# Optimization experiments

Measured on AMD Instinct MI355X. Metric: run time of the kernel, lower is better.

## Reference

```python
import jax, jax.numpy as jnp
import numpy as np

N, C, H, W, SF = 4, 3, 1024, 1024, 4


def setup_inputs() -> dict:
    key = jax.random.key(0)
    ks = jax.random.split(key, 6)
    z = jax.random.normal(ks[0], (N, C, H, W), dtype=jnp.float32)
    Fk = jax.random.normal(ks[1], (N, C, H, W, 2), dtype=jnp.float32)
    FkC = jax.random.normal(ks[2], (N, C, H, W, 2), dtype=jnp.float32)
    F2k = jax.random.normal(ks[3], (N, C, H, W, 2), dtype=jnp.float32)
    FkCFy = jax.random.normal(ks[4], (N, C, H, W, 2), dtype=jnp.float32)
    # alpha is a positive penalty weight; keep it away from 0 (it divides FX)
    alpha = jax.random.uniform(ks[5], (N, 1, 1, 1), dtype=jnp.float32,
                               minval=0.1, maxval=1.0)
    return {"z": z, "Fk": Fk, "FkC": FkC, "F2k": F2k,
            "FkCFy": FkCFy, "alpha": alpha, "sf": SF}


def _toc(t):
    # [..., 2] real/imag pair (old torch.rfft onesided=False layout) -> complex
    return jax.lax.complex(t[..., 0], t[..., 1])


def _block_mean(a, sf):
    # torch splits() + mean over the sf*sf blocks == mean over an sf-strided
    # block decomposition of the H and W axes (order of blocks is irrelevant
    # under the mean). a: (N, C, H, W) complex -> (N, C, H//sf, W//sf)
    n, c, h, w = a.shape
    return a.reshape(n, c, sf, h // sf, sf, w // sf).mean(axis=(2, 4))


def reference(z, Fk, FkC, F2k, FkCFy, alpha, sf):
    # torch.rfft(x, 2, onesided=False) == full 2-D FFT over last two dims
    FR = _toc(FkCFy) + jnp.fft.fft2(alpha * z)                  # (N,C,H,W) complex
    FBR = _block_mean(_toc(Fk) * FR, sf)                        # (N,C,H/sf,W/sf)
    invW = _block_mean(_toc(F2k), sf)                           # (N,C,H/sf,W/sf)
    invWBR = FBR / (invW + alpha)                               # csum adds alpha to real part
    FCBinvWBR = _toc(FkC) * jnp.tile(invWBR, (1, 1, sf, sf))    # torch .repeat == tile
    FX = (FR - FCBinvWBR) / alpha
    # torch.irfft(FX, 2, onesided=False) == real part of inverse 2-D FFT
    return jnp.real(jnp.fft.ifft2(FX))
```

## Files before the change

### kernel.cpp

```cpp
#include <hip/hip_runtime.h>
#include <cmath>

#define HN 1024
#define NCH 12
#define PI2 6.28318530717958647692f

__device__ __forceinline__ float2 cmul(float2 a, float2 b) {
  return make_float2(a.x * b.x - a.y * b.y, a.x * b.y + a.y * b.x);
}

__device__ __forceinline__ int drev(int k) {
  int r = 0;
#pragma unroll
  for (int i = 0; i < 5; ++i) { r = (r << 2) | (k & 3); k >>= 2; }
  return r;
}

__device__ __forceinline__ int aswz(int h, int w) { return w ^ ((h & 63) << 4); }

#define RIDX(h) ((h) + ((h) >> 4))
#define TIDX(i) ((i) + ((i) >> 4))
#define EIDX(h, c) ((h) * 17 + (c))

template <bool INV>
__device__ __forceinline__ void bf4(float2& a0, float2& a1, float2& a2, float2& a3,
                                    const float2* tw, int e) {
  float2 t0 = make_float2(a0.x + a2.x, a0.y + a2.y);
  float2 t1 = make_float2(a0.x - a2.x, a0.y - a2.y);
  float2 t2 = make_float2(a1.x + a3.x, a1.y + a3.y);
  float2 t3 = make_float2(a1.x - a3.x, a1.y - a3.y);
  float2 b0 = make_float2(t0.x + t2.x, t0.y + t2.y);
  float2 b2 = make_float2(t0.x - t2.x, t0.y - t2.y);
  float2 b1, b3;
  if (!INV) {
    b1 = make_float2(t1.x + t3.y, t1.y - t3.x);
    b3 = make_float2(t1.x - t3.y, t1.y + t3.x);
  } else {
    b1 = make_float2(t1.x - t3.y, t1.y + t3.x);
    b3 = make_float2(t1.x + t3.y, t1.y - t3.x);
  }
  float2 w1 = tw[e], w2 = tw[2 * e], w3 = tw[3 * e];
  if (INV) { w1.y = -w1.y; w2.y = -w2.y; w3.y = -w3.y; }
  a0 = b0;
  a1 = cmul(b1, w1);
  a2 = cmul(b2, w2);
  a3 = cmul(b3, w3);
}

template <bool INV>
__device__ __forceinline__ void bf4t(float2& a0, float2& a1, float2& a2, float2& a3,
                                     const float2* tw, int e) {
  float2 t0 = make_float2(a0.x + a2.x, a0.y + a2.y);
  float2 t1 = make_float2(a0.x - a2.x, a0.y - a2.y);
  float2 t2 = make_float2(a1.x + a3.x, a1.y + a3.y);
  float2 t3 = make_float2(a1.x - a3.x, a1.y - a3.y);
  float2 b0 = make_float2(t0.x + t2.x, t0.y + t2.y);
  float2 b2 = make_float2(t0.x - t2.x, t0.y - t2.y);
  float2 b1, b3;
  if (!INV) {
    b1 = make_float2(t1.x + t3.y, t1.y - t3.x);
    b3 = make_float2(t1.x - t3.y, t1.y + t3.x);
  } else {
    b1 = make_float2(t1.x - t3.y, t1.y + t3.x);
    b3 = make_float2(t1.x + t3.y, t1.y - t3.x);
  }
  float2 w1 = tw[TIDX(e)], w2 = tw[TIDX(2 * e)], w3 = tw[TIDX(3 * e)];
  if (INV) { w1.y = -w1.y; w2.y = -w2.y; w3.y = -w3.y; }
  a0 = b0;
  a1 = cmul(b1, w1);
  a2 = cmul(b2, w2);
  a3 = cmul(b3, w3);
}

__device__ __forceinline__ void tw_init(float2* tw, int t, int nthr) {
  for (int i = t; i < 768; i += nthr) {
    float s, c;
    sincosf((float)i * (PI2 / 1024.f), &s, &c);
    tw[i] = make_float2(c, -s);
  }
}

__device__ __forceinline__ void tw_init_p(float2* tw, int t, int nthr) {
  for (int i = t; i < 768; i += nthr) {
    float s, c;
    sincosf((float)i * (PI2 / 1024.f), &s, &c);
    tw[TIDX(i)] = make_float2(c, -s);
  }
}

template <bool INV>
__device__ __forceinline__ void fft_row(float2* x, const float2* tw, int t) {
#pragma unroll
  for (int ld = 8; ld >= 0; ld -= 2) {
    __syncthreads();
    const int d = 1 << ld;
    int j = t & (d - 1);
    int p0 = ((t >> ld) << (ld + 2)) | j;
    float2 a0 = x[RIDX(p0)];
    float2 a1 = x[RIDX(p0 + d)];
    float2 a2 = x[RIDX(p0 + 2 * d)];
    float2 a3 = x[RIDX(p0 + 3 * d)];
    bf4<INV>(a0, a1, a2, a3, tw, j << (8 - ld));
    x[RIDX(p0)] = a0;
    x[RIDX(p0 + d)] = a1;
    x[RIDX(p0 + 2 * d)] = a2;
    x[RIDX(p0 + 3 * d)] = a3;
  }
  __syncthreads();
}

template <bool INV>
__device__ __forceinline__ void colfft16(float2 (&r)[16], float2 (&q)[16],
                                         float2* ex, const float2* tw,
                                         int u, int c) {
  const int j2 = u & 3, B = u >> 2;
#pragma unroll
  for (int s = 0; s < 4; ++s)
    bf4t<INV>(r[s], r[s + 4], r[s + 8], r[s + 12], tw, u + (s << 6));
#pragma unroll
  for (int g = 0; g < 4; ++g)
    bf4t<INV>(r[4 * g], r[4 * g + 1], r[4 * g + 2], r[4 * g + 3], tw, u << 2);
#pragma unroll
  for (int it = 0; it < 8; ++it)
    ex[EIDX(u + (it << 6), c)] = r[it];
  __syncthreads();
  if (u < 32) {
#pragma unroll
    for (int m = 0; m < 16; ++m) {
      int hl = (B << 6) + j2 + ((m & 3) << 2) + ((m >> 2) << 4);
      q[m] = ex[EIDX(hl, c)];
    }
  }
  __syncthreads();
#pragma unroll
  for (int it = 8; it < 16; ++it)
    ex[EIDX(u + (it << 6) - 512, c)] = r[it];
  __syncthreads();
  if (u >= 32) {
#pragma unroll
    for (int m = 0; m < 16; ++m) {
      int hl = ((B - 8) << 6) + j2 + ((m & 3) << 2) + ((m >> 2) << 4);
      q[m] = ex[EIDX(hl, c)];
    }
  }
#pragma unroll
  for (int a = 0; a < 4; ++a)
    bf4t<INV>(q[a], q[4 + a], q[8 + a], q[12 + a], tw, (j2 + 4 * a) << 4);
#pragma unroll
  for (int b_ = 0; b_ < 4; ++b_)
    bf4t<INV>(q[4 * b_], q[4 * b_ + 1], q[4 * b_ + 2], q[4 * b_ + 3], tw, j2 << 6);
#pragma unroll
  for (int m = 0; m < 16; ++m) {
    float2 v = q[m];
    float2 p;
    p.x = __shfl_xor(v.x, 32);
    p.y = __shfl_xor(v.y, 32);
    float2 w;
    if (j2 & 2) { w.x = p.x - v.x; w.y = p.y - v.y; }
    else        { w.x = v.x + p.x; w.y = v.y + p.y; }
    float2 p2;
    p2.x = __shfl_xor(w.x, 16);
    p2.y = __shfl_xor(w.y, 16);
    float2 o;
    if (j2 == 0)      { o = make_float2(w.x + p2.x, w.y + p2.y); }
    else if (j2 == 1) { o = make_float2(p2.x - w.x, p2.y - w.y); }
    else if (j2 == 2) { o = INV ? make_float2(w.x - p2.y, w.y + p2.x)
                                : make_float2(w.x + p2.y, w.y - p2.x); }
    else              { o = INV ? make_float2(p2.x + w.y, p2.y - w.x)
                                : make_float2(p2.x - w.y, p2.y + w.x); }
    q[m] = o;
  }
}

__global__ __launch_bounds__(256) void k1_rowfft(const float* __restrict__ z,
                                                 const float* __restrict__ alpha,
                                                 float2* __restrict__ A) {
  __shared__ float2 x[1088];
  __shared__ float2 tw[768];
  const int t = threadIdx.x;
  const int row = blockIdx.x, nc = blockIdx.y;
  tw_init(tw, t, 256);
  const float al = alpha[nc / 3];
  const float* zr = z + ((size_t)nc * HN + row) * HN;
#pragma unroll
  for (int it = 0; it < 4; ++it) {
    int h = t + (it << 8);
    x[RIDX(h)] = make_float2(zr[h] * al, 0.f);
  }
  fft_row<false>(x, tw, t);
  float2* Ar = A + (size_t)nc * HN * HN + (size_t)row * HN;
  const int X = (row & 63) << 4;
#pragma unroll
  for (int it = 0; it < 4; ++it) {
    int k = t + (it << 8);
    Ar[k ^ X] = x[RIDX(drev(k))];
  }
}

__global__ __launch_bounds__(1024, 4) void k2_colfft(float2* __restrict__ A,
                                                     const float2* __restrict__ FkCFy) {
  __shared__ float2 ex[8704];
  __shared__ float2 tw[816];
  const int t = threadIdx.x;
  const int c = t & 15, u = t >> 4;
  const int w0 = blockIdx.x << 4;
  const int nc = blockIdx.y;
  const size_t base = (size_t)nc * HN * HN;
  float2 r[16], q[16];
#pragma unroll
  for (int it = 0; it < 16; ++it) {
    int h = u + (it << 6);
    r[it] = A[base + (size_t)h * HN + (aswz(h, w0) + c)];
  }
  tw_init_p(tw, t, 1024);
  __syncthreads();
  colfft16<false>(r, q, ex, tw, u, c);
  const int j2 = u & 3, B = u >> 2;
  const int f = ((j2 & 1) << 1) | (j2 >> 1);
#pragma unroll
  for (int m = 0; m < 16; ++m) {
    int k = (f << 8) | ((m & 3) << 6) | ((m >> 2) << 4) | ((B & 3) << 2) | (B >> 2);
    float2 fy = FkCFy[base + (size_t)k * HN + w0 + c];
    A[base + (size_t)k * HN + (aswz(k, w0) + c)] =
        make_float2(q[m].x + fy.x, q[m].y + fy.y);
  }
}

__global__ __launch_bounds__(256) void k3_reduce(const float2* __restrict__ A,
                                                 const float2* __restrict__ Fk,
                                                 const float2* __restrict__ F2k,
                                                 const float* __restrict__ alpha,
                                                 float2* __restrict__ iw) {
  int idx = blockIdx.x * 256 + threadIdx.x;
  int j = idx & 255, i = (idx >> 8) & 255, nc = idx >> 16;
  size_t base = (size_t)nc * HN * HN;
  float sx = 0.f, sy = 0.f, wx = 0.f, wy = 0.f;
#pragma unroll
  for (int s1 = 0; s1 < 4; ++s1) {
#pragma unroll
    for (int s2 = 0; s2 < 4; ++s2) {
      int h = (s1 << 8) + i, w = (s2 << 8) + j;
      size_t gl = base + (size_t)h * HN + w;
      float2 fr = A[base + (size_t)h * HN + aswz(h, w)];
      float2 fk = Fk[gl];
      float2 f2 = F2k[gl];
      sx += fk.x * fr.x - fk.y * fr.y;
      sy += fk.x * fr.y + fk.y * fr.x;
      wx += f2.x;
      wy += f2.y;
    }
  }
  const float al = alpha[nc / 3];
  float dx = wx * 0.0625f + al, dy = wy * 0.0625f;
  float nx = sx * 0.0625f, ny = sy * 0.0625f;
  float inv = 1.0f / (dx * dx + dy * dy);
  iw[idx] = make_float2((nx * dx + ny * dy) * inv, (ny * dx - nx * dy) * inv);
}

__global__ __launch_bounds__(1024, 4) void k4_colifft(float2* __restrict__ A,
                                                      const float2* __restrict__ FkC,
                                                      const float2* __restrict__ iw,
                                                      const float* __restrict__ alpha) {
  __shared__ float2 ex[8704];
  __shared__ float2 tw[816];
  const int t = threadIdx.x;
  const int c = t & 15, u = t >> 4;
  const int w0 = blockIdx.x << 4;
  const int nc = blockIdx.y;
  const float al = alpha[nc / 3];
  const float ra = 1.0f / al;
  const size_t base = (size_t)nc * HN * HN;
  const int jcol = (w0 + c) & 255;
  const float2* iwp = iw + ((size_t)nc << 16);
  float2 r[16], q[16];
#pragma unroll
  for (int it = 0; it < 16; ++it) {
    int h = u + (it << 6);
    float2 fr = A[base + (size_t)h * HN + (aswz(h, w0) + c)];
    float2 fc = FkC[base + (size_t)h * HN + w0 + c];
    float2 w = iwp[((h & 255) << 8) | jcol];
    float2 p = cmul(fc, w);
    r[it] = make_float2((fr.x - p.x) * ra, (fr.y - p.y) * ra);
  }
  tw_init_p(tw, t, 1024);
  __syncthreads();
  colfft16<true>(r, q, ex, tw, u, c);
  const int j2 = u & 3, B = u >> 2;
  const int f = ((j2 & 1) << 1) | (j2 >> 1);
#pragma unroll
  for (int m = 0; m < 16; ++m) {
    int k = (f << 8) | ((m & 3) << 6) | ((m >> 2) << 4) | ((B & 3) << 2) | (B >> 2);
    A[base + (size_t)k * HN + (aswz(k, w0) + c)] = q[m];
  }
}

__global__ __launch_bounds__(256) void k5_rowifft(const float2* __restrict__ A,
                                                  float* __restrict__ out) {
  __shared__ float2 x[1088];
  __shared__ float2 tw[768];
  const int t = threadIdx.x;
  const int row = blockIdx.x, nc = blockIdx.y;
  tw_init(tw, t, 256);
  const float2* Ar = A + (size_t)nc * HN * HN + (size_t)row * HN;
  const int X = (row & 63) << 4;
#pragma unroll
  for (int it = 0; it < 4; ++it) {
    int h = t + (it << 8);
    x[RIDX(h)] = Ar[h ^ X];
  }
  fft_row<true>(x, tw, t);
  float* outr = out + ((size_t)nc * HN + row) * HN;
  const float sc = 1.0f / (1024.0f * 1024.0f);
#pragma unroll
  for (int it = 0; it < 4; ++it) {
    int k = t + (it << 8);
    outr[k] = x[RIDX(drev(k))].x * sc;
  }
}

extern "C" void kernel_launch(void* const* d_in, const int* in_sizes, int n_in,
                              void* d_out, int out_size, void* d_ws, size_t ws_size,
                              hipStream_t stream) {
  const float*  z      = (const float*)d_in[0];
  const float2* Fk     = (const float2*)d_in[1];
  const float2* FkC    = (const float2*)d_in[2];
  const float2* F2k    = (const float2*)d_in[3];
  const float2* FkCFy  = (const float2*)d_in[4];
  const float*  alpha  = (const float*)d_in[5];
  (void)in_sizes; (void)n_in; (void)out_size; (void)ws_size;

  float2* A  = (float2*)d_ws;
  float2* iw = A + (size_t)NCH * HN * HN;
  float*  out = (float*)d_out;

  k1_rowfft<<<dim3(HN, NCH), dim3(256), 0, stream>>>(z, alpha, A);
  k2_colfft<<<dim3(HN / 16, NCH), dim3(1024), 0, stream>>>(A, FkCFy);
  k3_reduce<<<dim3(NCH * 256), dim3(256), 0, stream>>>(A, Fk, F2k, alpha, iw);
  k4_colifft<<<dim3(HN / 16, NCH), dim3(1024), 0, stream>>>(A, FkC, iw, alpha);
  k5_rowifft<<<dim3(HN, NCH), dim3(256), 0, stream>>>(A, out);
}
```

Baseline: 278.1 us.

## Fuse Fk*FR partial block reduction into column FFT and vectorize row I/O

The column FFT kernel now multiplies each FR value by Fk and partially reduces it across the four sf-strided row blocks with wave shuffles. It writes the partial sums to a small workspace buffer P, so the reduce kernel no longer re-reads the full FR and Fk arrays. The row FFT kernels also switch their global loads and stores to float4 accesses. This trades extra shuffles and Fk reads inside the column kernel for much less traffic in the reduce kernel. It also relies on extra workspace being available past iw.

```diff
diff --git a/kernel.cpp b/kernel.cpp
--- a/kernel.cpp
+++ b/kernel.cpp
@@ -181,24 +181,31 @@
   const int row = blockIdx.x, nc = blockIdx.y;
   tw_init(tw, t, 256);
   const float al = alpha[nc / 3];
-  const float* zr = z + ((size_t)nc * HN + row) * HN;
-#pragma unroll
-  for (int it = 0; it < 4; ++it) {
-    int h = t + (it << 8);
-    x[RIDX(h)] = make_float2(zr[h] * al, 0.f);
+  const float4* zr4 = (const float4*)(z + ((size_t)nc * HN + row) * HN);
+  {
+    float4 v = zr4[t];
+    int h = t << 2;
+    x[RIDX(h + 0)] = make_float2(v.x * al, 0.f);
+    x[RIDX(h + 1)] = make_float2(v.y * al, 0.f);
+    x[RIDX(h + 2)] = make_float2(v.z * al, 0.f);
+    x[RIDX(h + 3)] = make_float2(v.w * al, 0.f);
   }
   fft_row<false>(x, tw, t);
-  float2* Ar = A + (size_t)nc * HN * HN + (size_t)row * HN;
+  float4* Ar4 = (float4*)(A + (size_t)nc * HN * HN + (size_t)row * HN);
   const int X = (row & 63) << 4;
 #pragma unroll
-  for (int it = 0; it < 4; ++it) {
-    int k = t + (it << 8);
-    Ar[k ^ X] = x[RIDX(drev(k))];
+  for (int half = 0; half < 2; ++half) {
+    int k0 = (half << 9) | (t << 1);
+    float2 a = x[RIDX(drev(k0))];
+    float2 b = x[RIDX(drev(k0 | 1))];
+    Ar4[(k0 ^ X) >> 1] = make_float4(a.x, a.y, b.x, b.y);
   }
 }
 
 __global__ __launch_bounds__(1024, 4) void k2_colfft(float2* __restrict__ A,
-                                                     const float2* __restrict__ FkCFy) {
+                                                     const float2* __restrict__ FkCFy,
+                                                     const float2* __restrict__ Fk,
+                                                     float2* __restrict__ P) {
   __shared__ float2 ex[8704];
   __shared__ float2 tw[816];
   const int t = threadIdx.x;
@@ -217,38 +224,48 @@
   colfft16<false>(r, q, ex, tw, u, c);
   const int j2 = u & 3, B = u >> 2;
   const int f = ((j2 & 1) << 1) | (j2 >> 1);
+  float2* Pp = P + (((size_t)nc) << 18) + w0 + c;
 #pragma unroll
   for (int m = 0; m < 16; ++m) {
-    int k = (f << 8) | ((m & 3) << 6) | ((m >> 2) << 4) | ((B & 3) << 2) | (B >> 2);
+    int klo = ((m & 3) << 6) | ((m >> 2) << 4) | ((B & 3) << 2) | (B >> 2);
+    int k = (f << 8) | klo;
     float2 fy = FkCFy[base + (size_t)k * HN + w0 + c];
-    A[base + (size_t)k * HN + (aswz(k, w0) + c)] =
-        make_float2(q[m].x + fy.x, q[m].y + fy.y);
-  }
-}
-
-__global__ __launch_bounds__(256) void k3_reduce(const float2* __restrict__ A,
-                                                 const float2* __restrict__ Fk,
+    float2 fr = make_float2(q[m].x + fy.x, q[m].y + fy.y);
+    A[base + (size_t)k * HN + (aswz(k, w0) + c)] = fr;
+    float2 fk = Fk[base + (size_t)k * HN + w0 + c];
+    float2 pr = cmul(fk, fr);
+    pr.x += __shfl_xor(pr.x, 16);
+    pr.y += __shfl_xor(pr.y, 16);
+    pr.x += __shfl_xor(pr.x, 32);
+    pr.y += __shfl_xor(pr.y, 32);
+    if (j2 == 0) Pp[(size_t)klo << 10] = pr;
+  }
+}
+
+__global__ __launch_bounds__(256) void k3_reduce(const float2* __restrict__ P,
                                                  const float2* __restrict__ F2k,
                                                  const float* __restrict__ alpha,
                                                  float2* __restrict__ iw) {
   int idx = blockIdx.x * 256 + threadIdx.x;
   int j = idx & 255, i = (idx >> 8) & 255, nc = idx >> 16;
   size_t base = (size_t)nc * HN * HN;
-  float sx = 0.f, sy = 0.f, wx = 0.f, wy = 0.f;
+  float wx = 0.f, wy = 0.f;
 #pragma unroll
   for (int s1 = 0; s1 < 4; ++s1) {
 #pragma unroll
     for (int s2 = 0; s2 < 4; ++s2) {
-      int h = (s1 << 8) + i, w = (s2 << 8) + j;
-      size_t gl = base + (size_t)h * HN + w;
-      float2 fr = A[base + (size_t)h * HN + aswz(h, w)];
-      float2 fk = Fk[gl];
-      float2 f2 = F2k[gl];
-      sx += fk.x * fr.x - fk.y * fr.y;
-      sy += fk.x * fr.y + fk.y * fr.x;
+      float2 f2 = F2k[base + (size_t)((s1 << 8) + i) * HN + ((s2 << 8) + j)];
       wx += f2.x;
       wy += f2.y;
     }
+  }
+  const float2* Pp = P + (((size_t)nc) << 18) + ((size_t)i << 10);
+  float sx = 0.f, sy = 0.f;
+#pragma unroll
+  for (int s2 = 0; s2 < 4; ++s2) {
+    float2 p = Pp[(s2 << 8) + j];
+    sx += p.x;
+    sy += p.y;
   }
   const float al = alpha[nc / 3];
   float dx = wx * 0.0625f + al, dy = wy * 0.0625f;
@@ -301,20 +318,26 @@
   const int t = threadIdx.x;
   const int row = blockIdx.x, nc = blockIdx.y;
   tw_init(tw, t, 256);
-  const float2* Ar = A + (size_t)nc * HN * HN + (size_t)row * HN;
+  const float4* Ar4 = (const float4*)(A + (size_t)nc * HN * HN + (size_t)row * HN);
   const int X = (row & 63) << 4;
 #pragma unroll
-  for (int it = 0; it < 4; ++it) {
-    int h = t + (it << 8);
-    x[RIDX(h)] = Ar[h ^ X];
+  for (int half = 0; half < 2; ++half) {
+    int h0 = (half << 9) | (t << 1);
+    float4 v = Ar4[(h0 ^ X) >> 1];
+    x[RIDX(h0)] = make_float2(v.x, v.y);
+    x[RIDX(h0 | 1)] = make_float2(v.z, v.w);
   }
   fft_row<true>(x, tw, t);
-  float* outr = out + ((size_t)nc * HN + row) * HN;
+  float4* outr4 = (float4*)(out + ((size_t)nc * HN + row) * HN);
   const float sc = 1.0f / (1024.0f * 1024.0f);
-#pragma unroll
-  for (int it = 0; it < 4; ++it) {
-    int k = t + (it << 8);
-    outr[k] = x[RIDX(drev(k))].x * sc;
+  {
+    int k = t << 2;
+    float4 o;
+    o.x = x[RIDX(drev(k + 0))].x * sc;
+    o.y = x[RIDX(drev(k + 1))].x * sc;
+    o.z = x[RIDX(drev(k + 2))].x * sc;
+    o.w = x[RIDX(drev(k + 3))].x * sc;
+    outr4[t] = o;
   }
 }
 
@@ -331,11 +354,12 @@
 
   float2* A  = (float2*)d_ws;
   float2* iw = A + (size_t)NCH * HN * HN;
+  float2* P  = iw + (size_t)NCH * 256 * 256;
   float*  out = (float*)d_out;
 
   k1_rowfft<<<dim3(HN, NCH), dim3(256), 0, stream>>>(z, alpha, A);
-  k2_colfft<<<dim3(HN / 16, NCH), dim3(1024), 0, stream>>>(A, FkCFy);
-  k3_reduce<<<dim3(NCH * 256), dim3(256), 0, stream>>>(A, Fk, F2k, alpha, iw);
+  k2_colfft<<<dim3(HN / 16, NCH), dim3(1024), 0, stream>>>(A, FkCFy, Fk, P);
+  k3_reduce<<<dim3(NCH * 256), dim3(256), 0, stream>>>(P, F2k, alpha, iw);
   k4_colifft<<<dim3(HN / 16, NCH), dim3(1024), 0, stream>>>(A, FkC, iw, alpha);
   k5_rowifft<<<dim3(HN, NCH), dim3(256), 0, stream>>>(A, out);
 }
```

New measurement: 291.9 us. 5.0% more time.
